# Optimization experiments

Hardware: AMD Instinct MI355X
Metric: run time of the kernel (lower is better)

The kernel has to match this reference:

```python
import jax, jax.numpy as jnp
import numpy as np

DIM, B, H, W = 96, 2, 64, 64
D_INNER, D_STATE, DT_RANK, K = 2 * DIM, 16, 6, 4


def _conv2d(x, w, b=None, padding=0, dilation=1, groups=1):
    out = jax.lax.conv_general_dilated(
        x, w, (1, 1), [(padding, padding)] * 2,
        rhs_dilation=(dilation, dilation),
        dimension_numbers=('NCHW', 'OIHW', 'NCHW'),
        feature_group_count=groups)
    return out if b is None else out + b[None, :, None, None]


def _layernorm(x, g, b, eps=1e-5):
    mu = x.mean(-1, keepdims=True)
    xc = x - mu
    var = (xc * xc).mean(-1, keepdims=True)
    return xc * jax.lax.rsqrt(var + eps) * g + b


def _chan_recal(t, w1, w2):
    s = t.mean((2, 3)) + t.max(axis=(2, 3))          # GAP + GMP, (B,C)
    w = jax.nn.sigmoid(jax.nn.relu(s @ w1.T) @ w2.T)
    return t * w[:, :, None, None]


def _selective_scan(u, delta, A, Bm, Cm, D):
    # u, delta: (B,K,d,L); A: (K,d,N); Bm,Cm: (B,K,N,L); D: (K,d)
    Bsz, Kk, d, L = u.shape
    N = A.shape[-1]
    seq = (jnp.moveaxis(delta, -1, 0), jnp.moveaxis(u, -1, 0),
           jnp.moveaxis(Bm, -1, 0), jnp.moveaxis(Cm, -1, 0))
    h0 = jnp.zeros((Bsz, Kk, d, N), u.dtype)

    def step(h, inp):
        dl, ul, bl, cl = inp  # (B,K,d),(B,K,d),(B,K,N),(B,K,N)
        h = jnp.exp(dl[..., None] * A) * h + (dl * ul)[..., None] * bl[:, :, None, :]
        return h, (h * cl[:, :, None, :]).sum(-1)

    _, ys = jax.lax.scan(step, h0, seq)
    return jnp.moveaxis(ys, 0, -1) + D[None, :, :, None] * u  # (B,K,d,L)


def _ss2d(x, in_proj_w, conv_w, conv_b, x_proj_w, dt_w, dt_b,
          A_logs, Ds, out_norm_g, out_norm_b, out_proj_w):
    Bsz, Hh, Ww, C = x.shape
    d = in_proj_w.shape[0] // 2
    xm, z = jnp.split(x @ in_proj_w.T, 2, axis=-1)
    xm = jnp.transpose(xm, (0, 3, 1, 2))  # (B,d,H,W)
    xm = jax.nn.silu(_conv2d(xm, conv_w, conv_b, padding=1, groups=d))
    L = Hh * Ww
    x_hw = xm.reshape(Bsz, d, L)
    x_wh = jnp.transpose(xm, (0, 1, 3, 2)).reshape(Bsz, d, L)
    xs = jnp.stack([x_hw, x_wh, x_hw[..., ::-1], x_wh[..., ::-1]], axis=1)  # (B,4,d,L)
    x_dbl = jnp.einsum('bkdl,kcd->bkcl', xs, x_proj_w)
    r = dt_w.shape[-1]
    N = A_logs.shape[-1]
    dts, Bs, Cs = jnp.split(x_dbl, [r, r + N], axis=2)
    dts = jax.nn.softplus(jnp.einsum('bkrl,kdr->bkdl', dts, dt_w) + dt_b[None, :, :, None])
    out_y = _selective_scan(xs, dts, -jnp.exp(A_logs), Bs, Cs, Ds)
    inv_y = out_y[:, 2:4, :, ::-1]
    wh = lambda t: jnp.transpose(t.reshape(Bsz, d, Ww, Hh), (0, 1, 3, 2)).reshape(Bsz, d, L)
    y = out_y[:, 0] + inv_y[:, 0] + wh(out_y[:, 1]) + wh(inv_y[:, 1])
    y = _layernorm(jnp.transpose(y, (0, 2, 1)).reshape(Bsz, Hh, Ww, d), out_norm_g, out_norm_b)
    return (y * jax.nn.silu(z)) @ out_proj_w.T


def _forward(x, arf_w1, arf_b1, arf_w2, arf_b2, arf_w3, arf_b3, arf_w4, arf_b4,
             fuse_w, fuse_b, edge_w, enh_w1, enh_b1, bn_g, bn_b, enh_w2, enh_b2,
             pre_fc1, pre_fc2, norm_g, norm_b, in_proj_w, ss_conv_w, ss_conv_b,
             x_proj_w, dt_w, dt_b, A_logs, Ds, out_norm_g, out_norm_b, out_proj_w,
             post_fc1, post_fc2, proj_w, proj_b):
    shortcut = x
    C = x.shape[1]
    g = C // 4
    # AdaptiveReceptiveField (fc gating branch is dead code in the original forward)
    f1 = _conv2d(x, arf_w1, arf_b1, padding=1, dilation=1, groups=g)
    f2 = _conv2d(x, arf_w2, arf_b2, padding=2, dilation=2, groups=g)
    f3 = _conv2d(x, arf_w3, arf_b3, padding=4, dilation=4, groups=g)
    f4 = _conv2d(x, arf_w4, arf_b4, padding=8, dilation=8, groups=g)
    h = _conv2d(jnp.concatenate([f1, f2, f3, f4], 1), fuse_w, fuse_b)
    # LearnableEdgeEnhancement (BatchNorm in training mode: batch stats, biased var)
    edge = _conv2d(h, edge_w, None, padding=1, groups=C)
    e = _conv2d(edge, enh_w1, enh_b1)
    mu = e.mean((0, 2, 3), keepdims=True)
    var = ((e - mu) ** 2).mean((0, 2, 3), keepdims=True)
    e = jax.nn.relu((e - mu) * jax.lax.rsqrt(var + 1e-5) * bn_g[None, :, None, None]
                    + bn_b[None, :, None, None])
    h = h * (1.0 + jax.nn.sigmoid(_conv2d(e, enh_w2, enh_b2)))
    h = _chan_recal(h, pre_fc1, pre_fc2)
    hn = _layernorm(jnp.transpose(h, (0, 2, 3, 1)), norm_g, norm_b)
    hn = _ss2d(hn, in_proj_w, ss_conv_w, ss_conv_b, x_proj_w, dt_w, dt_b,
               A_logs, Ds, out_norm_g, out_norm_b, out_proj_w)
    h = jnp.transpose(hn, (0, 3, 1, 2))
    h = _chan_recal(h, post_fc1, post_fc2)
    h = _conv2d(h, proj_w, proj_b)
    return shortcut + h


def setup_inputs():
    key = jax.random.key(0)
    ks = iter(jax.random.split(key, 48))
    rn = lambda shape, s=0.05: jax.random.normal(next(ks), shape, jnp.float32) * s
    lap = jnp.array([[0., 1., 0.], [1., -4., 1.], [0., 1., 0.]], jnp.float32)
    q = DIM // 4
    inp = {
        'x': jax.random.normal(next(ks), (B, DIM, H, W), jnp.float32),
        'arf_w1': rn((q, 4, 3, 3)), 'arf_b1': rn((q,)),
        'arf_w2': rn((q, 4, 3, 3)), 'arf_b2': rn((q,)),
        'arf_w3': rn((q, 4, 3, 3)), 'arf_b3': rn((q,)),
        'arf_w4': rn((q, 4, 3, 3)), 'arf_b4': rn((q,)),
        'fuse_w': rn((DIM, DIM, 1, 1)), 'fuse_b': rn((DIM,)),
        'edge_w': jnp.tile(lap[None, None], (DIM, 1, 1, 1)),
        'enh_w1': rn((q, DIM, 1, 1)), 'enh_b1': rn((q,)),
        'bn_g': jnp.ones((q,), jnp.float32), 'bn_b': jnp.zeros((q,), jnp.float32),
        'enh_w2': rn((DIM, q, 1, 1)), 'enh_b2': rn((DIM,)),
        'pre_fc1': rn((q, DIM)), 'pre_fc2': rn((DIM, q)),
        'norm_g': jnp.ones((DIM,), jnp.float32), 'norm_b': jnp.zeros((DIM,), jnp.float32),
        'in_proj_w': rn((2 * D_INNER, DIM)),
        'ss_conv_w': rn((D_INNER, 1, 3, 3)), 'ss_conv_b': rn((D_INNER,)),
        'x_proj_w': rn((K, DT_RANK + 2 * D_STATE, D_INNER)),
        'dt_w': rn((K, D_INNER, DT_RANK), 0.1), 'dt_b': rn((K, D_INNER), 0.1),
        'A_logs': jnp.broadcast_to(jnp.log(jnp.arange(1, D_STATE + 1, dtype=jnp.float32)),
                                   (K, D_INNER, D_STATE)) + jnp.zeros((K, D_INNER, D_STATE), jnp.float32),
        'Ds': jnp.ones((K, D_INNER), jnp.float32),
        'out_norm_g': jnp.ones((D_INNER,), jnp.float32),
        'out_norm_b': jnp.zeros((D_INNER,), jnp.float32),
        'out_proj_w': rn((DIM, D_INNER)),
        'post_fc1': rn((q, DIM)), 'post_fc2': rn((DIM, q)),
        'proj_w': rn((DIM, DIM, 1, 1)), 'proj_b': rn((DIM,)),
    }
    return inp


def reference(x, arf_w1, arf_b1, arf_w2, arf_b2, arf_w3, arf_b3, arf_w4, arf_b4,
              fuse_w, fuse_b, edge_w, enh_w1, enh_b1, bn_g, bn_b, enh_w2, enh_b2,
              pre_fc1, pre_fc2, norm_g, norm_b, in_proj_w, ss_conv_w, ss_conv_b,
              x_proj_w, dt_w, dt_b, A_logs, Ds, out_norm_g, out_norm_b, out_proj_w,
              post_fc1, post_fc2, proj_w, proj_b):
    return _forward(x, arf_w1, arf_b1, arf_w2, arf_b2, arf_w3, arf_b3, arf_w4, arf_b4,
                    fuse_w, fuse_b, edge_w, enh_w1, enh_b1, bn_g, bn_b, enh_w2, enh_b2,
                    pre_fc1, pre_fc2, norm_g, norm_b, in_proj_w, ss_conv_w, ss_conv_b,
                    x_proj_w, dt_w, dt_b, A_logs, Ds, out_norm_g, out_norm_b, out_proj_w,
                    post_fc1, post_fc2, proj_w, proj_b)
```

## Files before the change

kernel.cpp:

```cpp
#include <hip/hip_runtime.h>
#include <cmath>

#define LL   4096
#define HWD  64
#define CCH  96
#define QQ   24
#define DDI  192
#define NST  16
#define NCH  128
#define CLEN 32
#define TSC  32
#define XT2  32
#define XP   108
#define FP   100
#define VP   204

static const size_t OFF_F   = 0;
static const size_t OFF_H   = 786432;
static const size_t OFF_E   = 1572864;
static const size_t OFF_BN  = 1769472;
static const size_t OFF_XM  = 2556736;
static const size_t OFF_Z   = 4129600;
static const size_t OFF_XC  = 5702464;
static const size_t OFF_DTS = 7275328;
static const size_t OFF_BC  = 13566784;
static const size_t OFF_YK  = 14615360;
static const size_t OFF_Y2  = 22528832;
static const size_t OFF_HL  = 23315264;
static const size_t OFF_SD  = 26460992;
static const size_t OFF_HIN = 26657600;
static const size_t OFF_S1PS= 29803328;
static const size_t OFF_S1PM= 29806400;
static const size_t OFF_S2PS= 29809472;
static const size_t OFF_S2PM= 29821760;

static __device__ __forceinline__ int map_k(int k, int l) {
  int ll = (k & 2) ? (LL - 1 - l) : l;
  return (k & 1) ? (((ll & 63) << 6) | (ll >> 6)) : ll;
}

__global__ __launch_bounds__(256) void k_arf(const float* __restrict__ x,
    const float* __restrict__ w1, const float* __restrict__ b1,
    const float* __restrict__ w2, const float* __restrict__ b2,
    const float* __restrict__ w3, const float* __restrict__ b3,
    const float* __restrict__ w4, const float* __restrict__ b4,
    float* __restrict__ f) {
  int idx = blockIdx.x * 256 + threadIdx.x;
  int p = idx & (LL - 1);
  int oc = __builtin_amdgcn_readfirstlane((idx >> 12) % CCH);
  int b  = __builtin_amdgcn_readfirstlane(idx / (CCH * LL));
  int i = oc / QQ, q = oc % QQ;
  int dil = 1 << i;
  const float* w  = (i == 0 ? w1 : i == 1 ? w2 : i == 2 ? w3 : w4) + q * 36;
  const float* bb = (i == 0 ? b1 : i == 1 ? b2 : i == 2 ? b3 : b4);
  int yy0 = p >> 6, xx0 = p & 63;
  float acc = bb[q];
  const float* xin = x + ((size_t)b * CCH + q * 4) * LL;
  #pragma unroll
  for (int ky = 0; ky < 3; ky++) {
    int yy = yy0 + (ky - 1) * dil;
    if (yy < 0 || yy >= HWD) continue;
    #pragma unroll
    for (int kx = 0; kx < 3; kx++) {
      int xx = xx0 + (kx - 1) * dil;
      if (xx < 0 || xx >= HWD) continue;
      int pp = (yy << 6) + xx;
      #pragma unroll
      for (int ci = 0; ci < 4; ci++)
        acc += w[ci * 9 + ky * 3 + kx] * xin[(size_t)ci * LL + pp];
    }
  }
  f[idx] = acc;
}

__global__ __launch_bounds__(256) void k_fuse(const float* __restrict__ f,
    const float* __restrict__ fw, const float* __restrict__ fb, float* __restrict__ h) {
  int pix0 = blockIdx.x * 64;
  int oc0 = blockIdx.y * 48;
  int b = pix0 >> 12, p0 = pix0 & (LL - 1);
  int t = threadIdx.x;
  __shared__ float fs[64][FP];
  __shared__ float wbuf[48 * 96];
  for (int i = t; i < 96 * 16; i += 256) {
    int c = i >> 4, q = i & 15;
    float4 v = *(const float4*)(f + ((size_t)b * CCH + c) * LL + p0 + q * 4);
    fs[q * 4 + 0][c] = v.x; fs[q * 4 + 1][c] = v.y;
    fs[q * 4 + 2][c] = v.z; fs[q * 4 + 3][c] = v.w;
  }
  {
    const float4* src = (const float4*)(fw + (size_t)oc0 * CCH);
    float4* dst = (float4*)wbuf;
    for (int i = t; i < 48 * 24; i += 256) dst[i] = src[i];
  }
  __syncthreads();
  int px = t & 63;
  int cg = __builtin_amdgcn_readfirstlane(t >> 6);
  float acc[12];
  #pragma unroll
  for (int j = 0; j < 12; j++) acc[j] = 0.f;
  for (int c4 = 0; c4 < 24; c4++) {
    float4 xv = *(const float4*)(&fs[px][c4 * 4]);
    #pragma unroll
    for (int j = 0; j < 12; j++) {
      float4 wv = *(const float4*)(&wbuf[(cg * 12 + j) * 96 + c4 * 4]);
      acc[j] = fmaf(xv.x, wv.x, fmaf(xv.y, wv.y, fmaf(xv.z, wv.z, fmaf(xv.w, wv.w, acc[j]))));
    }
  }
  __syncthreads();
  float* ot = &fs[0][0];
  #pragma unroll
  for (int j = 0; j < 12; j++) ot[px * 49 + cg * 12 + j] = acc[j];
  __syncthreads();
  for (int i = t; i < 48 * 64; i += 256) {
    int o = i >> 6, p2 = i & 63;
    h[((size_t)b * CCH + oc0 + o) * LL + p0 + p2] = ot[p2 * 49 + o] + fb[oc0 + o];
  }
}

__global__ __launch_bounds__(256) void k_edge(const float* __restrict__ h,
    const float* __restrict__ ew, float* __restrict__ edge) {
  int idx = blockIdx.x * 256 + threadIdx.x;
  int p = idx & (LL - 1);
  int c = __builtin_amdgcn_readfirstlane((idx >> 12) % CCH);
  int b = __builtin_amdgcn_readfirstlane(idx / (CCH * LL));
  int yy0 = p >> 6, xx0 = p & 63;
  const float* w = ew + c * 9;
  const float* hr = h + ((size_t)b * CCH + c) * LL;
  float acc = 0.f;
  #pragma unroll
  for (int ky = 0; ky < 3; ky++) {
    int yy = yy0 + ky - 1;
    if (yy < 0 || yy >= HWD) continue;
    #pragma unroll
    for (int kx = 0; kx < 3; kx++) {
      int xx = xx0 + kx - 1;
      if (xx < 0 || xx >= HWD) continue;
      acc += w[ky * 3 + kx] * hr[(yy << 6) + xx];
    }
  }
  edge[idx] = acc;
}

__global__ __launch_bounds__(256) void k_e1(const float* __restrict__ edge,
    const float* __restrict__ w, const float* __restrict__ bias, float* __restrict__ e) {
  int idx = blockIdx.x * 256 + threadIdx.x;
  int p = idx & (LL - 1);
  int q = __builtin_amdgcn_readfirstlane((idx >> 12) % QQ);
  int b = __builtin_amdgcn_readfirstlane(idx / (QQ * LL));
  const float* er = edge + (size_t)b * CCH * LL + p;
  const float* wr = w + q * CCH;
  float acc = bias[q];
  for (int c = 0; c < CCH; c++) acc += wr[c] * er[(size_t)c * LL];
  e[idx] = acc;
}

__global__ __launch_bounds__(256) void k_bnstats(const float* __restrict__ e,
    const float* __restrict__ g, const float* __restrict__ bb, float* __restrict__ bn) {
  int q = blockIdx.x, tid = threadIdx.x;
  __shared__ float rs[256], r2[256];
  float s = 0.f, s2 = 0.f;
  for (int b = 0; b < 2; b++) {
    const float* er = e + ((size_t)b * QQ + q) * LL;
    for (int p = tid; p < LL; p += 256) { float v = er[p]; s += v; s2 += v * v; }
  }
  rs[tid] = s; r2[tid] = s2; __syncthreads();
  for (int st = 128; st > 0; st >>= 1) {
    if (tid < st) { rs[tid] += rs[tid + st]; r2[tid] += r2[tid + st]; }
    __syncthreads();
  }
  if (tid == 0) {
    float mu = rs[0] / (2.f * LL);
    float var = r2[0] / (2.f * LL) - mu * mu;
    float sc = g[q] * rsqrtf(var + 1e-5f);
    bn[q] = sc;
    bn[QQ + q] = bb[q] - mu * sc;
  }
}

__global__ __launch_bounds__(256) void k_enh(const float* __restrict__ e,
    const float* __restrict__ bn, const float* __restrict__ w2,
    const float* __restrict__ b2, float* __restrict__ h,
    float* __restrict__ s1ps, float* __restrict__ s1pm) {
  int tid = threadIdx.x;
  int idx = blockIdx.x * 256 + tid;
  int p = idx & (LL - 1);
  int o = __builtin_amdgcn_readfirstlane((idx >> 12) % CCH);
  int b = __builtin_amdgcn_readfirstlane(idx / (CCH * LL));
  const float* er = e + (size_t)b * QQ * LL + p;
  const float* wr = w2 + o * QQ;
  float acc = b2[o];
  #pragma unroll
  for (int q = 0; q < QQ; q++) {
    float en = fmaxf(er[(size_t)q * LL] * bn[q] + bn[QQ + q], 0.f);
    acc += wr[q] * en;
  }
  float sig = 1.f / (1.f + __expf(-acc));
  float val = h[idx] * (1.f + sig);
  h[idx] = val;
  __shared__ float rsum[256], rmax[256];
  rsum[tid] = val; rmax[tid] = val; __syncthreads();
  for (int st = 128; st > 0; st >>= 1) {
    if (tid < st) { rsum[tid] += rsum[tid + st]; rmax[tid] = fmaxf(rmax[tid], rmax[tid + st]); }
    __syncthreads();
  }
  if (tid == 0) {
    int row = blockIdx.x >> 4, blk = blockIdx.x & 15;
    s1ps[row * 16 + blk] = rsum[0];
    s1pm[row * 16 + blk] = rmax[0];
  }
}

__global__ __launch_bounds__(256) void k_inproj(const float* __restrict__ h,
    const float* __restrict__ s1ps, const float* __restrict__ s1pm,
    const float* __restrict__ fc1, const float* __restrict__ fc2,
    const float* __restrict__ ng, const float* __restrict__ nb,
    const float* __restrict__ W, float* __restrict__ xm, float* __restrict__ z) {
  int pix0 = blockIdx.x * 64;
  int oc0 = blockIdx.y * CCH;
  int b = pix0 >> 12, p0 = pix0 & (LL - 1);
  int t = threadIdx.x;
  __shared__ float xs[64][XP];
  __shared__ float wbuf[CCH * CCH];
  __shared__ float wsm[CCH];
  __shared__ float hid[QQ];
  __shared__ float ps[64][4], ps2[64][4];
  __shared__ float mu_s[64], rs_s[64];
  if (t < CCH) {
    const float4* sp = (const float4*)(s1ps + (size_t)(b * CCH + t) * 16);
    const float4* mp = (const float4*)(s1pm + (size_t)(b * CCH + t) * 16);
    float s = 0.f, m = -3.402823466e38f;
    #pragma unroll
    for (int i = 0; i < 4; i++) {
      float4 a = sp[i]; s += a.x + a.y + a.z + a.w;
      float4 c = mp[i]; m = fmaxf(m, fmaxf(fmaxf(c.x, c.y), fmaxf(c.z, c.w)));
    }
    wsm[t] = s / (float)LL + m;
  }
  __syncthreads();
  if (t < QQ) {
    float a = 0.f;
    for (int c = 0; c < CCH; c++) a += wsm[c] * fc1[t * CCH + c];
    hid[t] = fmaxf(a, 0.f);
  }
  __syncthreads();
  float w1v = 0.f;
  if (t < CCH) {
    float a = 0.f;
    #pragma unroll
    for (int q = 0; q < QQ; q++) a += hid[q] * fc2[t * QQ + q];
    w1v = 1.f / (1.f + __expf(-a));
  }
  __syncthreads();
  if (t < CCH) wsm[t] = w1v;
  {
    const float4* src = (const float4*)(W + (size_t)oc0 * CCH);
    float4* dst = (float4*)wbuf;
    for (int i = t; i < CCH * 24; i += 256) dst[i] = src[i];
  }
  __syncthreads();
  for (int i = t; i < CCH * 16; i += 256) {
    int c = i >> 4, q = i & 15;
    float w = wsm[c];
    float4 v = *(const float4*)(h + ((size_t)b * CCH + c) * LL + p0 + q * 4);
    xs[q * 4 + 0][c] = v.x * w; xs[q * 4 + 1][c] = v.y * w;
    xs[q * 4 + 2][c] = v.z * w; xs[q * 4 + 3][c] = v.w * w;
  }
  __syncthreads();
  {
    int px = t & 63, qr = t >> 6;
    float s = 0.f, s2 = 0.f;
    #pragma unroll
    for (int j = 0; j < 24; j++) { float v = xs[px][qr * 24 + j]; s += v; s2 += v * v; }
    ps[px][qr] = s; ps2[px][qr] = s2;
  }
  __syncthreads();
  if (t < 64) {
    float ss = ps[t][0] + ps[t][1] + ps[t][2] + ps[t][3];
    float ss2 = ps2[t][0] + ps2[t][1] + ps2[t][2] + ps2[t][3];
    float mu = ss / (float)CCH;
    mu_s[t] = mu;
    rs_s[t] = rsqrtf(ss2 / (float)CCH - mu * mu + 1e-5f);
  }
  __syncthreads();
  for (int i = t; i < 64 * CCH; i += 256) {
    int px = i / CCH, c = i % CCH;
    xs[px][c] = (xs[px][c] - mu_s[px]) * rs_s[px] * ng[c] + nb[c];
  }
  __syncthreads();
  int li = t & 63;
  int cg = __builtin_amdgcn_readfirstlane(t >> 6);
  float acc[24];
  #pragma unroll
  for (int j = 0; j < 24; j++) acc[j] = 0.f;
  for (int dq = 0; dq < 24; dq++) {
    float4 xv = *(const float4*)(&xs[li][dq * 4]);
    #pragma unroll
    for (int j = 0; j < 24; j++) {
      float4 wv = *(const float4*)(&wbuf[(cg + 4 * j) * CCH + dq * 4]);
      acc[j] = fmaf(xv.x, wv.x, fmaf(xv.y, wv.y, fmaf(xv.z, wv.z, fmaf(xv.w, wv.w, acc[j]))));
    }
  }
  __syncthreads();
  float* ot = &xs[0][0];
  #pragma unroll
  for (int j = 0; j < 24; j++) ot[li * 97 + cg + 4 * j] = acc[j];
  __syncthreads();
  float* dst = (oc0 < DDI) ? xm : z;
  int od0 = oc0 % DDI;
  for (int i = t; i < 64 * 96; i += 256) {
    int row = i / 96, c = i % 96;
    dst[(size_t)(pix0 + row) * DDI + od0 + c] = ot[row * 97 + c];
  }
}

__global__ __launch_bounds__(256) void k_ssconv(const float* __restrict__ xm,
    const float* __restrict__ w, const float* __restrict__ bias, float* __restrict__ xc) {
  int idx = blockIdx.x * 256 + threadIdx.x;
  int d = idx % DDI;
  int rem = idx / DDI;
  int xx0 = rem & 63;
  int y0 = ((rem >> 6) & 31) * 2;
  int b = idx / (DDI * LL / 2);
  float wv[9];
  #pragma unroll
  for (int i = 0; i < 9; i++) wv[i] = w[d * 9 + i];
  float acc0 = bias[d], acc1 = bias[d];
  const float* xr = xm + (size_t)b * LL * DDI + d;
  #pragma unroll
  for (int ky = -1; ky <= 2; ky++) {
    int yy = y0 + ky;
    if (yy < 0 || yy >= HWD) continue;
    #pragma unroll
    for (int kx = -1; kx <= 1; kx++) {
      int xx = xx0 + kx;
      if (xx < 0 || xx >= HWD) continue;
      float val = xr[(size_t)((yy << 6) + xx) * DDI];
      if (ky <= 1) acc0 += wv[(ky + 1) * 3 + (kx + 1)] * val;
      if (ky >= 0) acc1 += wv[ky * 3 + (kx + 1)] * val;
    }
  }
  size_t o0 = ((size_t)b * LL + (y0 << 6) + xx0) * DDI + d;
  xc[o0] = acc0 / (1.f + __expf(-acc0));
  xc[o0 + 64 * DDI] = acc1 / (1.f + __expf(-acc1));
}

__global__ __launch_bounds__(256) void k_xdbl(const float* __restrict__ xc,
    const float* __restrict__ xpw, float* __restrict__ dtr_ws, float* __restrict__ bcb) {
  int lt = blockIdx.x;
  int bk = blockIdx.y;
  int b = bk >> 2, k = bk & 3;
  int t = threadIdx.x;
  __shared__ float xs[XT2][XP];
  __shared__ float wbuf[38 * 96];
  int l0 = lt * XT2;
  int pos = t & 31;
  int cg = t >> 5;
  float acc[5];
  #pragma unroll
  for (int j = 0; j < 5; j++) acc[j] = 0.f;
  for (int h = 0; h < 2; h++) {
    __syncthreads();
    for (int i = t; i < XT2 * 24; i += 256) {
      int row = i / 24, dq = i % 24;
      int p = map_k(k, l0 + row);
      *(float4*)(&xs[row][dq * 4]) =
          *(const float4*)(xc + ((size_t)b * LL + p) * DDI + h * 96 + dq * 4);
    }
    for (int i = t; i < 38 * 24; i += 256) {
      int c = i / 24, dq = i % 24;
      *(float4*)(&wbuf[c * 96 + dq * 4]) =
          *(const float4*)(xpw + ((size_t)k * 38 + c) * DDI + h * 96 + dq * 4);
    }
    __syncthreads();
    for (int dq = 0; dq < 24; dq++) {
      float4 xv = *(const float4*)(&xs[pos][dq * 4]);
      #pragma unroll
      for (int j = 0; j < 5; j++) {
        int c = cg + 8 * j;
        if (c < 38) {
          float4 wv = *(const float4*)(&wbuf[c * 96 + dq * 4]);
          acc[j] = fmaf(xv.x, wv.x, fmaf(xv.y, wv.y, fmaf(xv.z, wv.z, fmaf(xv.w, wv.w, acc[j]))));
        }
      }
    }
  }
  #pragma unroll
  for (int j = 0; j < 5; j++) {
    int c = cg + 8 * j;
    if (c < 6) dtr_ws[((size_t)bk * LL + l0 + pos) * 6 + c] = acc[j];
    else if (c < 38) bcb[((size_t)bk * LL + l0 + pos) * 32 + (c - 6)] = acc[j];
  }
}

template <int PASS>
__global__ __launch_bounds__(192) void k_scan(const float* __restrict__ dtr_ws,
    const float* __restrict__ bcb, const float* __restrict__ xc,
    const float* __restrict__ A_logs, const float* __restrict__ dtw,
    const float* __restrict__ dtb, float* __restrict__ hl, float* __restrict__ sd,
    const float* __restrict__ hin, float* __restrict__ yk) {
  int ch = blockIdx.x, bk = blockIdx.y;
  int b = bk >> 2, k = bk & 3;
  int d = threadIdx.x;
  __shared__ float u_s[TSC][DDI];
  __shared__ float bcs[TSC][32];
  __shared__ float dtr_s[TSC][6];
  float Av[NST];
  #pragma unroll
  for (int n = 0; n < NST; n++) Av[n] = -__expf(A_logs[(size_t)(k * DDI + d) * NST + n]);
  bool pw = true;
  #pragma unroll
  for (int n = 1; n < NST; n++) pw = pw && (fabsf(Av[n] - (float)(n + 1) * Av[0]) <= 1e-3f * (n + 1));
  float wdt[6];
  #pragma unroll
  for (int r = 0; r < 6; r++) wdt[r] = dtw[((size_t)(k * DDI + d)) * 6 + r];
  float bdt = dtb[k * DDI + d];
  float h[NST];
  if (PASS == 0) {
    #pragma unroll
    for (int n = 0; n < NST; n++) h[n] = 0.f;
  } else {
    const float* hp = hin + ((size_t)(bk * DDI + d) * NCH + ch) * NST;
    #pragma unroll
    for (int n = 0; n < NST; n++) h[n] = hp[n];
  }
  float sumdt = 0.f;
  int l0 = ch * CLEN;
  {
    for (int i = d; i < TSC * (DDI / 4); i += 192) {
      int row = i / (DDI / 4), q = i % (DDI / 4);
      int p = map_k(k, l0 + row);
      ((float4*)u_s)[i] = *(const float4*)(xc + ((size_t)b * LL + p) * DDI + q * 4);
    }
    {
      const float4* src = (const float4*)(bcb + ((size_t)bk * LL + l0) * 32);
      float4* dst = (float4*)bcs;
      for (int i = d; i < TSC * 32 / 4; i += 192) dst[i] = src[i];
    }
    for (int i = d; i < TSC * 6; i += 192)
      ((float*)dtr_s)[i] = dtr_ws[((size_t)bk * LL + l0) * 6 + i];
    __syncthreads();
    for (int tt = 0; tt < TSC; tt++) {
      float a = bdt;
      #pragma unroll
      for (int r = 0; r < 6; r++) a = fmaf(wdt[r], dtr_s[tt][r], a);
      float dt = (a > 15.f) ? a : __logf(1.f + __expf(a));
      float u  = u_s[tt][d];
      float dtu = dt * u;
      if (PASS == 0) sumdt += dt;
      float eA[NST];
      if (pw) {
        float E = __expf(dt * Av[0]);
        float en = 1.f;
        #pragma unroll
        for (int n = 0; n < NST; n++) { en *= E; eA[n] = en; }
      } else {
        #pragma unroll
        for (int n = 0; n < NST; n++) eA[n] = __expf(dt * Av[n]);
      }
      float y = 0.f;
      #pragma unroll
      for (int n = 0; n < NST; n++) {
        h[n] = eA[n] * h[n] + dtu * bcs[tt][n];
        y += h[n] * bcs[tt][16 + n];
      }
      if (PASS == 1) {
        int p = map_k(k, l0 + tt);
        yk[((size_t)bk * LL + p) * DDI + d] = y;
      }
    }
  }
  if (PASS == 0) {
    float* hp = hl + ((size_t)(bk * DDI + d) * NCH + ch) * NST;
    #pragma unroll
    for (int n = 0; n < NST; n++) hp[n] = h[n];
    sd[(size_t)(bk * DDI + d) * NCH + ch] = sumdt;
  }
}

__global__ __launch_bounds__(256) void k_carry(const float* __restrict__ A_logs,
    const float* __restrict__ hl, const float* __restrict__ sd, float* __restrict__ hin) {
  int idx = blockIdx.x * 256 + threadIdx.x;
  int n = idx & 15;
  int d = (idx >> 4) % DDI;
  int bk = idx / (DDI * NST);
  int k = bk & 3;
  float Aval = -__expf(A_logs[(size_t)(k * DDI + d) * NST + n]);
  float h = 0.f;
  size_t base = (size_t)(bk * DDI + d) * NCH;
  for (int ch = 0; ch < NCH; ch++) {
    hin[(base + ch) * NST + n] = h;
    h = __expf(Aval * sd[base + ch]) * h + hl[(base + ch) * NST + n];
  }
}

__global__ __launch_bounds__(256) void k_outproj(const float* __restrict__ yk,
    const float* __restrict__ xc, const float* __restrict__ Ds, const float* __restrict__ z,
    const float* __restrict__ ong, const float* __restrict__ onb,
    const float* __restrict__ W, float* __restrict__ y2,
    float* __restrict__ s2ps, float* __restrict__ s2pm) {
  int pix0 = blockIdx.x * 64;
  int oc0 = blockIdx.y * 48;
  int b = pix0 >> 12, p0 = pix0 & (LL - 1);
  int t = threadIdx.x;
  __shared__ float xs[64][VP];
  __shared__ float wbuf[48 * 96];
  __shared__ float dsum[DDI];
  __shared__ float ps[64][4], ps2[64][4];
  __shared__ float mu_s[64], rs_s[64];
  if (t < 48) {
    float4 a  = *(const float4*)(Ds + t * 4);
    float4 c1 = *(const float4*)(Ds + DDI + t * 4);
    float4 c2 = *(const float4*)(Ds + 2 * DDI + t * 4);
    float4 c3 = *(const float4*)(Ds + 3 * DDI + t * 4);
    *(float4*)(&dsum[t * 4]) = make_float4(a.x + c1.x + c2.x + c3.x, a.y + c1.y + c2.y + c3.y,
                                           a.z + c1.z + c2.z + c3.z, a.w + c1.w + c2.w + c3.w);
  }
  __syncthreads();
  int px = t & 63, qr = t >> 6;
  int p = p0 + px;
  size_t pb = ((size_t)b * LL + p) * DDI;
  size_t yb = ((size_t)b * 4 * LL + p) * DDI;
  {
    float s = 0.f, s2 = 0.f;
    #pragma unroll
    for (int j = 0; j < 12; j++) {
      int c = (qr * 12 + j) * 4;
      float4 y0 = *(const float4*)(yk + yb + c);
      float4 y1 = *(const float4*)(yk + yb + (size_t)LL * DDI + c);
      float4 y2v = *(const float4*)(yk + yb + 2ul * LL * DDI + c);
      float4 y3 = *(const float4*)(yk + yb + 3ul * LL * DDI + c);
      float4 u = *(const float4*)(xc + pb + c);
      float4 dv = *(const float4*)(&dsum[c]);
      float4 v;
      v.x = y0.x + y1.x + y2v.x + y3.x + dv.x * u.x;
      v.y = y0.y + y1.y + y2v.y + y3.y + dv.y * u.y;
      v.z = y0.z + y1.z + y2v.z + y3.z + dv.z * u.z;
      v.w = y0.w + y1.w + y2v.w + y3.w + dv.w * u.w;
      *(float4*)(&xs[px][c]) = v;
      s += v.x + v.y + v.z + v.w;
      s2 += v.x * v.x + v.y * v.y + v.z * v.z + v.w * v.w;
    }
    ps[px][qr] = s; ps2[px][qr] = s2;
  }
  __syncthreads();
  if (t < 64) {
    float ss = ps[t][0] + ps[t][1] + ps[t][2] + ps[t][3];
    float ss2 = ps2[t][0] + ps2[t][1] + ps2[t][2] + ps2[t][3];
    float mu = ss / (float)DDI;
    mu_s[t] = mu;
    rs_s[t] = rsqrtf(ss2 / (float)DDI - mu * mu + 1e-5f);
  }
  __syncthreads();
  {
    float mu = mu_s[px], rs = rs_s[px];
    #pragma unroll
    for (int j = 0; j < 12; j++) {
      int c = (qr * 12 + j) * 4;
      float4 v = *(const float4*)(&xs[px][c]);
      float4 zz = *(const float4*)(z + pb + c);
      float4 og = *(const float4*)(ong + c);
      float4 ob = *(const float4*)(onb + c);
      float4 gv;
      gv.x = ((v.x - mu) * rs * og.x + ob.x) * (zz.x / (1.f + __expf(-zz.x)));
      gv.y = ((v.y - mu) * rs * og.y + ob.y) * (zz.y / (1.f + __expf(-zz.y)));
      gv.z = ((v.z - mu) * rs * og.z + ob.z) * (zz.z / (1.f + __expf(-zz.z)));
      gv.w = ((v.w - mu) * rs * og.w + ob.w) * (zz.w / (1.f + __expf(-zz.w)));
      *(float4*)(&xs[px][c]) = gv;
    }
  }
  int li = px;
  int cg = __builtin_amdgcn_readfirstlane(qr);
  float acc[12];
  #pragma unroll
  for (int j = 0; j < 12; j++) acc[j] = 0.f;
  for (int hh = 0; hh < 2; hh++) {
    __syncthreads();
    for (int i = t; i < 48 * 24; i += 256) {
      int c = i / 24, dq = i % 24;
      *(float4*)(&wbuf[c * 96 + dq * 4]) =
          *(const float4*)(W + (size_t)(oc0 + c) * DDI + hh * 96 + dq * 4);
    }
    __syncthreads();
    for (int dq = 0; dq < 24; dq++) {
      float4 xv = *(const float4*)(&xs[li][hh * 96 + dq * 4]);
      #pragma unroll
      for (int j = 0; j < 12; j++) {
        float4 wv = *(const float4*)(&wbuf[(cg + 4 * j) * 96 + dq * 4]);
        acc[j] = fmaf(xv.x, wv.x, fmaf(xv.y, wv.y, fmaf(xv.z, wv.z, fmaf(xv.w, wv.w, acc[j]))));
      }
    }
  }
  int lane = t & 63;
  #pragma unroll
  for (int j = 0; j < 12; j++) {
    float sv = acc[j], mv = acc[j];
    #pragma unroll
    for (int o = 32; o > 0; o >>= 1) {
      sv += __shfl_xor(sv, o);
      mv = fmaxf(mv, __shfl_xor(mv, o));
    }
    if (lane == 0) {
      int oc = oc0 + cg + 4 * j;
      int tile = blockIdx.x & 63;
      s2ps[(size_t)(b * CCH + oc) * 64 + tile] = sv;
      s2pm[(size_t)(b * CCH + oc) * 64 + tile] = mv;
    }
  }
  __syncthreads();
  float* ot = &xs[0][0];
  #pragma unroll
  for (int j = 0; j < 12; j++) ot[li * 49 + cg + 4 * j] = acc[j];
  __syncthreads();
  for (int i = t; i < 48 * 64; i += 256) {
    int o = i / 64, pi = i % 64;
    y2[((size_t)b * CCH + oc0 + o) * LL + p0 + pi] = ot[pi * 49 + o];
  }
}

__global__ __launch_bounds__(256) void k_final(const float* __restrict__ x,
    const float* __restrict__ y2, const float* __restrict__ s2ps, const float* __restrict__ s2pm,
    const float* __restrict__ fc1, const float* __restrict__ fc2,
    const float* __restrict__ pw, const float* __restrict__ pb, float* __restrict__ out) {
  int pix0 = blockIdx.x * 64;
  int oc0 = blockIdx.y * 48;
  int b = pix0 >> 12, p0 = pix0 & (LL - 1);
  int t = threadIdx.x;
  __shared__ float fs[64][FP];
  __shared__ float wbuf[48 * 96];
  __shared__ float wsm[CCH];
  __shared__ float hid[QQ];
  if (t < CCH) {
    const float4* sp = (const float4*)(s2ps + (size_t)(b * CCH + t) * 64);
    const float4* mp = (const float4*)(s2pm + (size_t)(b * CCH + t) * 64);
    float s = 0.f, m = -3.402823466e38f;
    #pragma unroll
    for (int i = 0; i < 16; i++) {
      float4 a = sp[i]; s += a.x + a.y + a.z + a.w;
      float4 c = mp[i]; m = fmaxf(m, fmaxf(fmaxf(c.x, c.y), fmaxf(c.z, c.w)));
    }
    wsm[t] = s / (float)LL + m;
  }
  __syncthreads();
  if (t < QQ) {
    float a = 0.f;
    for (int c = 0; c < CCH; c++) a += wsm[c] * fc1[t * CCH + c];
    hid[t] = fmaxf(a, 0.f);
  }
  __syncthreads();
  float w2v = 0.f;
  if (t < CCH) {
    float a = 0.f;
    #pragma unroll
    for (int q = 0; q < QQ; q++) a += hid[q] * fc2[t * QQ + q];
    w2v = 1.f / (1.f + __expf(-a));
  }
  __syncthreads();
  if (t < CCH) wsm[t] = w2v;
  __syncthreads();
  for (int i = t; i < 96 * 16; i += 256) {
    int c = i >> 4, q = i & 15;
    float4 v = *(const float4*)(y2 + ((size_t)b * CCH + c) * LL + p0 + q * 4);
    fs[q * 4 + 0][c] = v.x; fs[q * 4 + 1][c] = v.y;
    fs[q * 4 + 2][c] = v.z; fs[q * 4 + 3][c] = v.w;
  }
  for (int i = t; i < 48 * 24; i += 256) {
    int row = i / 24, q = i % 24;
    float4 wv = *(const float4*)(pw + (size_t)(oc0 + row) * CCH + q * 4);
    ((float4*)wbuf)[i] = make_float4(wv.x * wsm[q * 4], wv.y * wsm[q * 4 + 1],
                                     wv.z * wsm[q * 4 + 2], wv.w * wsm[q * 4 + 3]);
  }
  __syncthreads();
  int px = t & 63;
  int cg = __builtin_amdgcn_readfirstlane(t >> 6);
  float acc[12];
  #pragma unroll
  for (int j = 0; j < 12; j++) acc[j] = 0.f;
  for (int c4 = 0; c4 < 24; c4++) {
    float4 xv = *(const float4*)(&fs[px][c4 * 4]);
    #pragma unroll
    for (int j = 0; j < 12; j++) {
      float4 wv = *(const float4*)(&wbuf[(cg * 12 + j) * 96 + c4 * 4]);
      acc[j] = fmaf(xv.x, wv.x, fmaf(xv.y, wv.y, fmaf(xv.z, wv.z, fmaf(xv.w, wv.w, acc[j]))));
    }
  }
  __syncthreads();
  float* ot = &fs[0][0];
  #pragma unroll
  for (int j = 0; j < 12; j++) ot[px * 49 + cg * 12 + j] = acc[j];
  __syncthreads();
  for (int i = t; i < 48 * 64; i += 256) {
    int o = i >> 6, p2 = i & 63;
    size_t oi = ((size_t)b * CCH + oc0 + o) * LL + p0 + p2;
    out[oi] = x[oi] + pb[oc0 + o] + ot[p2 * 49 + o];
  }
}

extern "C" void kernel_launch(void* const* d_in, const int* in_sizes, int n_in,
                              void* d_out, int out_size, void* d_ws, size_t ws_size,
                              hipStream_t stream) {
  const float* x        = (const float*)d_in[0];
  const float* arf_w1   = (const float*)d_in[1];
  const float* arf_b1   = (const float*)d_in[2];
  const float* arf_w2   = (const float*)d_in[3];
  const float* arf_b2   = (const float*)d_in[4];
  const float* arf_w3   = (const float*)d_in[5];
  const float* arf_b3   = (const float*)d_in[6];
  const float* arf_w4   = (const float*)d_in[7];
  const float* arf_b4   = (const float*)d_in[8];
  const float* fuse_w   = (const float*)d_in[9];
  const float* fuse_b   = (const float*)d_in[10];
  const float* edge_w   = (const float*)d_in[11];
  const float* enh_w1   = (const float*)d_in[12];
  const float* enh_b1   = (const float*)d_in[13];
  const float* bn_g     = (const float*)d_in[14];
  const float* bn_b     = (const float*)d_in[15];
  const float* enh_w2   = (const float*)d_in[16];
  const float* enh_b2   = (const float*)d_in[17];
  const float* pre_fc1  = (const float*)d_in[18];
  const float* pre_fc2  = (const float*)d_in[19];
  const float* norm_g   = (const float*)d_in[20];
  const float* norm_b   = (const float*)d_in[21];
  const float* in_proj_w= (const float*)d_in[22];
  const float* ss_conv_w= (const float*)d_in[23];
  const float* ss_conv_b= (const float*)d_in[24];
  const float* x_proj_w = (const float*)d_in[25];
  const float* dt_w     = (const float*)d_in[26];
  const float* dt_b     = (const float*)d_in[27];
  const float* A_logs   = (const float*)d_in[28];
  const float* Ds       = (const float*)d_in[29];
  const float* out_ng   = (const float*)d_in[30];
  const float* out_nb   = (const float*)d_in[31];
  const float* out_proj_w = (const float*)d_in[32];
  const float* post_fc1 = (const float*)d_in[33];
  const float* post_fc2 = (const float*)d_in[34];
  const float* proj_w   = (const float*)d_in[35];
  const float* proj_b   = (const float*)d_in[36];

  float* ws = (float*)d_ws;
  float* fbuf  = ws + OFF_F;
  float* hbuf  = ws + OFF_H;
  float* ebuf  = ws + OFF_E;
  float* bnbuf = ws + OFF_BN;
  float* xmbuf = ws + OFF_XM;
  float* zbuf  = ws + OFF_Z;
  float* xcbuf = ws + OFF_XC;
  float* dtrbuf= ws + OFF_DTS;
  float* bcbuf = ws + OFF_BC;
  float* ykbuf = ws + OFF_YK;
  float* y2buf = ws + OFF_Y2;
  float* hlbuf = ws + OFF_HL;
  float* sdbuf = ws + OFF_SD;
  float* hinbuf= ws + OFF_HIN;
  float* s1ps  = ws + OFF_S1PS;
  float* s1pm  = ws + OFF_S1PM;
  float* s2ps  = ws + OFF_S2PS;
  float* s2pm  = ws + OFF_S2PM;

  k_arf<<<3072, 256, 0, stream>>>(x, arf_w1, arf_b1, arf_w2, arf_b2, arf_w3, arf_b3, arf_w4, arf_b4, fbuf);
  k_fuse<<<dim3(128, 2), 256, 0, stream>>>(fbuf, fuse_w, fuse_b, hbuf);
  k_edge<<<3072, 256, 0, stream>>>(hbuf, edge_w, fbuf);
  k_e1<<<768, 256, 0, stream>>>(fbuf, enh_w1, enh_b1, ebuf);
  k_bnstats<<<24, 256, 0, stream>>>(ebuf, bn_g, bn_b, bnbuf);
  k_enh<<<3072, 256, 0, stream>>>(ebuf, bnbuf, enh_w2, enh_b2, hbuf, s1ps, s1pm);
  k_inproj<<<dim3(128, 4), 256, 0, stream>>>(hbuf, s1ps, s1pm, pre_fc1, pre_fc2, norm_g, norm_b, in_proj_w, xmbuf, zbuf);
  k_ssconv<<<3072, 256, 0, stream>>>(xmbuf, ss_conv_w, ss_conv_b, xcbuf);
  k_xdbl<<<dim3(LL / XT2, 8), 256, 0, stream>>>(xcbuf, x_proj_w, dtrbuf, bcbuf);
  k_scan<0><<<dim3(NCH, 8), 192, 0, stream>>>(dtrbuf, bcbuf, xcbuf, A_logs, dt_w, dt_b, hlbuf, sdbuf, nullptr, nullptr);
  k_carry<<<96, 256, 0, stream>>>(A_logs, hlbuf, sdbuf, hinbuf);
  k_scan<1><<<dim3(NCH, 8), 192, 0, stream>>>(dtrbuf, bcbuf, xcbuf, A_logs, dt_w, dt_b, nullptr, nullptr, hinbuf, ykbuf);
  k_outproj<<<dim3(128, 2), 256, 0, stream>>>(ykbuf, xcbuf, Ds, zbuf, out_ng, out_nb, out_proj_w, y2buf, s2ps, s2pm);
  k_final<<<dim3(128, 2), 256, 0, stream>>>(x, y2buf, s2ps, s2pm, post_fc1, post_fc2, proj_w, proj_b, (float*)d_out);
  (void)in_sizes; (void)n_in; (void)out_size; (void)ws_size;
}
```

Baseline: 228.9 us.

## Fuse chunked scan passes via cooperative grid sync and fold BN stats into producers

The two scan passes and the carry-propagation kernel are merged into one cooperative kernel that keeps the staged chunk inputs in shared memory and uses two grid-wide syncs in place of separate launches. The chunk data is loaded once instead of twice. The BN statistics kernel is removed: k_e1 now writes per-block partial sums, and each k_enh block reduces them into shared scale and shift values. Together these cut three kernel launches and one reload of the scan inputs. In exchange, the carry phase now runs on only 24576 of the 196608 scan threads, every k_enh block repeats the small stats reduction, and all 1024 blocks must be resident at once for the cooperative launch to work.

```diff
diff --git a/kernel.cpp b/kernel.cpp
--- a/kernel.cpp
+++ b/kernel.cpp
@@ -1,5 +1,8 @@
 #include <hip/hip_runtime.h>
+#include <hip/hip_cooperative_groups.h>
 #include <cmath>
+
+namespace cg = cooperative_groups;
 
 #define LL   4096
 #define HWD  64
@@ -15,24 +18,25 @@
 #define FP   100
 #define VP   204
 
-static const size_t OFF_F   = 0;
-static const size_t OFF_H   = 786432;
-static const size_t OFF_E   = 1572864;
-static const size_t OFF_BN  = 1769472;
-static const size_t OFF_XM  = 2556736;
-static const size_t OFF_Z   = 4129600;
-static const size_t OFF_XC  = 5702464;
-static const size_t OFF_DTS = 7275328;
-static const size_t OFF_BC  = 13566784;
-static const size_t OFF_YK  = 14615360;
-static const size_t OFF_Y2  = 22528832;
-static const size_t OFF_HL  = 23315264;
-static const size_t OFF_SD  = 26460992;
-static const size_t OFF_HIN = 26657600;
-static const size_t OFF_S1PS= 29803328;
-static const size_t OFF_S1PM= 29806400;
-static const size_t OFF_S2PS= 29809472;
-static const size_t OFF_S2PM= 29821760;
+static const size_t OFF_F    = 0;
+static const size_t OFF_H    = 786432;
+static const size_t OFF_E    = 1572864;
+static const size_t OFF_E1PS = 1769472;
+static const size_t OFF_E1P2 = 1770240;
+static const size_t OFF_XM   = 2556736;
+static const size_t OFF_Z    = 4129600;
+static const size_t OFF_XC   = 5702464;
+static const size_t OFF_DTS  = 7275328;
+static const size_t OFF_BC   = 13566784;
+static const size_t OFF_YK   = 14615360;
+static const size_t OFF_Y2   = 22528832;
+static const size_t OFF_HL   = 23315264;
+static const size_t OFF_SD   = 26460992;
+static const size_t OFF_HIN  = 26657600;
+static const size_t OFF_S1PS = 29803328;
+static const size_t OFF_S1PM = 29806400;
+static const size_t OFF_S2PS = 29809472;
+static const size_t OFF_S2PM = 29821760;
 
 static __device__ __forceinline__ int map_k(int k, int l) {
   int ll = (k & 2) ? (LL - 1 - l) : l;
@@ -94,7 +98,7 @@
   }
   __syncthreads();
   int px = t & 63;
-  int cg = __builtin_amdgcn_readfirstlane(t >> 6);
+  int cg2 = __builtin_amdgcn_readfirstlane(t >> 6);
   float acc[12];
   #pragma unroll
   for (int j = 0; j < 12; j++) acc[j] = 0.f;
@@ -102,14 +106,14 @@
     float4 xv = *(const float4*)(&fs[px][c4 * 4]);
     #pragma unroll
     for (int j = 0; j < 12; j++) {
-      float4 wv = *(const float4*)(&wbuf[(cg * 12 + j) * 96 + c4 * 4]);
+      float4 wv = *(const float4*)(&wbuf[(cg2 * 12 + j) * 96 + c4 * 4]);
       acc[j] = fmaf(xv.x, wv.x, fmaf(xv.y, wv.y, fmaf(xv.z, wv.z, fmaf(xv.w, wv.w, acc[j]))));
     }
   }
   __syncthreads();
   float* ot = &fs[0][0];
   #pragma unroll
-  for (int j = 0; j < 12; j++) ot[px * 49 + cg * 12 + j] = acc[j];
+  for (int j = 0; j < 12; j++) ot[px * 49 + cg2 * 12 + j] = acc[j];
   __syncthreads();
   for (int i = t; i < 48 * 64; i += 256) {
     int o = i >> 6, p2 = i & 63;
@@ -142,8 +146,10 @@
 }
 
 __global__ __launch_bounds__(256) void k_e1(const float* __restrict__ edge,
-    const float* __restrict__ w, const float* __restrict__ bias, float* __restrict__ e) {
-  int idx = blockIdx.x * 256 + threadIdx.x;
+    const float* __restrict__ w, const float* __restrict__ bias, float* __restrict__ e,
+    float* __restrict__ e1ps, float* __restrict__ e1p2) {
+  int tid = threadIdx.x;
+  int idx = blockIdx.x * 256 + tid;
   int p = idx & (LL - 1);
   int q = __builtin_amdgcn_readfirstlane((idx >> 12) % QQ);
   int b = __builtin_amdgcn_readfirstlane(idx / (QQ * LL));
@@ -152,36 +158,37 @@
   float acc = bias[q];
   for (int c = 0; c < CCH; c++) acc += wr[c] * er[(size_t)c * LL];
   e[idx] = acc;
-}
-
-__global__ __launch_bounds__(256) void k_bnstats(const float* __restrict__ e,
-    const float* __restrict__ g, const float* __restrict__ bb, float* __restrict__ bn) {
-  int q = blockIdx.x, tid = threadIdx.x;
   __shared__ float rs[256], r2[256];
-  float s = 0.f, s2 = 0.f;
-  for (int b = 0; b < 2; b++) {
-    const float* er = e + ((size_t)b * QQ + q) * LL;
-    for (int p = tid; p < LL; p += 256) { float v = er[p]; s += v; s2 += v * v; }
-  }
-  rs[tid] = s; r2[tid] = s2; __syncthreads();
+  rs[tid] = acc; r2[tid] = acc * acc; __syncthreads();
   for (int st = 128; st > 0; st >>= 1) {
     if (tid < st) { rs[tid] += rs[tid + st]; r2[tid] += r2[tid + st]; }
     __syncthreads();
   }
-  if (tid == 0) {
-    float mu = rs[0] / (2.f * LL);
-    float var = r2[0] / (2.f * LL) - mu * mu;
-    float sc = g[q] * rsqrtf(var + 1e-5f);
-    bn[q] = sc;
-    bn[QQ + q] = bb[q] - mu * sc;
-  }
+  if (tid == 0) { e1ps[blockIdx.x] = rs[0]; e1p2[blockIdx.x] = r2[0]; }
 }
 
 __global__ __launch_bounds__(256) void k_enh(const float* __restrict__ e,
-    const float* __restrict__ bn, const float* __restrict__ w2,
-    const float* __restrict__ b2, float* __restrict__ h,
-    float* __restrict__ s1ps, float* __restrict__ s1pm) {
+    const float* __restrict__ e1ps, const float* __restrict__ e1p2,
+    const float* __restrict__ bn_g, const float* __restrict__ bn_b,
+    const float* __restrict__ w2, const float* __restrict__ b2,
+    float* __restrict__ h, float* __restrict__ s1ps, float* __restrict__ s1pm) {
   int tid = threadIdx.x;
+  __shared__ float bns[QQ], bnsh[QQ];
+  if (tid < QQ) {
+    float s = 0.f, s2 = 0.f;
+    #pragma unroll
+    for (int b2 = 0; b2 < 2; b2++)
+      for (int i = 0; i < 16; i++) {
+        int pi = (b2 * QQ + tid) * 16 + i;
+        s += e1ps[pi]; s2 += e1p2[pi];
+      }
+    float mu = s / (2.f * LL);
+    float var = s2 / (2.f * LL) - mu * mu;
+    float sc = bn_g[tid] * rsqrtf(var + 1e-5f);
+    bns[tid] = sc;
+    bnsh[tid] = bn_b[tid] - mu * sc;
+  }
+  __syncthreads();
   int idx = blockIdx.x * 256 + tid;
   int p = idx & (LL - 1);
   int o = __builtin_amdgcn_readfirstlane((idx >> 12) % CCH);
@@ -191,7 +198,7 @@
   float acc = b2[o];
   #pragma unroll
   for (int q = 0; q < QQ; q++) {
-    float en = fmaxf(er[(size_t)q * LL] * bn[q] + bn[QQ + q], 0.f);
+    float en = fmaxf(er[(size_t)q * LL] * bns[q] + bnsh[q], 0.f);
     acc += wr[q] * en;
   }
   float sig = 1.f / (1.f + __expf(-acc));
@@ -288,7 +295,7 @@
   }
   __syncthreads();
   int li = t & 63;
-  int cg = __builtin_amdgcn_readfirstlane(t >> 6);
+  int cg2 = __builtin_amdgcn_readfirstlane(t >> 6);
   float acc[24];
   #pragma unroll
   for (int j = 0; j < 24; j++) acc[j] = 0.f;
@@ -296,14 +303,14 @@
     float4 xv = *(const float4*)(&xs[li][dq * 4]);
     #pragma unroll
     for (int j = 0; j < 24; j++) {
-      float4 wv = *(const float4*)(&wbuf[(cg + 4 * j) * CCH + dq * 4]);
+      float4 wv = *(const float4*)(&wbuf[(cg2 + 4 * j) * CCH + dq * 4]);
       acc[j] = fmaf(xv.x, wv.x, fmaf(xv.y, wv.y, fmaf(xv.z, wv.z, fmaf(xv.w, wv.w, acc[j]))));
     }
   }
   __syncthreads();
   float* ot = &xs[0][0];
   #pragma unroll
-  for (int j = 0; j < 24; j++) ot[li * 97 + cg + 4 * j] = acc[j];
+  for (int j = 0; j < 24; j++) ot[li * 97 + cg2 + 4 * j] = acc[j];
   __syncthreads();
   float* dst = (oc0 < DDI) ? xm : z;
   int od0 = oc0 % DDI;
@@ -354,7 +361,7 @@
   __shared__ float wbuf[38 * 96];
   int l0 = lt * XT2;
   int pos = t & 31;
-  int cg = t >> 5;
+  int cg2 = t >> 5;
   float acc[5];
   #pragma unroll
   for (int j = 0; j < 5; j++) acc[j] = 0.f;
@@ -376,7 +383,7 @@
       float4 xv = *(const float4*)(&xs[pos][dq * 4]);
       #pragma unroll
       for (int j = 0; j < 5; j++) {
-        int c = cg + 8 * j;
+        int c = cg2 + 8 * j;
         if (c < 38) {
           float4 wv = *(const float4*)(&wbuf[c * 96 + dq * 4]);
           acc[j] = fmaf(xv.x, wv.x, fmaf(xv.y, wv.y, fmaf(xv.z, wv.z, fmaf(xv.w, wv.w, acc[j]))));
@@ -386,18 +393,17 @@
   }
   #pragma unroll
   for (int j = 0; j < 5; j++) {
-    int c = cg + 8 * j;
+    int c = cg2 + 8 * j;
     if (c < 6) dtr_ws[((size_t)bk * LL + l0 + pos) * 6 + c] = acc[j];
     else if (c < 38) bcb[((size_t)bk * LL + l0 + pos) * 32 + (c - 6)] = acc[j];
   }
 }
 
-template <int PASS>
-__global__ __launch_bounds__(192) void k_scan(const float* __restrict__ dtr_ws,
+__global__ __launch_bounds__(192) void k_scan_all(const float* __restrict__ dtr_ws,
     const float* __restrict__ bcb, const float* __restrict__ xc,
     const float* __restrict__ A_logs, const float* __restrict__ dtw,
     const float* __restrict__ dtb, float* __restrict__ hl, float* __restrict__ sd,
-    const float* __restrict__ hin, float* __restrict__ yk) {
+    float* __restrict__ hin, float* __restrict__ yk) {
   int ch = blockIdx.x, bk = blockIdx.y;
   int b = bk >> 2, k = bk & 3;
   int d = threadIdx.x;
@@ -414,82 +420,98 @@
   #pragma unroll
   for (int r = 0; r < 6; r++) wdt[r] = dtw[((size_t)(k * DDI + d)) * 6 + r];
   float bdt = dtb[k * DDI + d];
+  int l0 = ch * CLEN;
+  for (int i = d; i < TSC * (DDI / 4); i += 192) {
+    int row = i / (DDI / 4), q = i % (DDI / 4);
+    int p = map_k(k, l0 + row);
+    ((float4*)u_s)[i] = *(const float4*)(xc + ((size_t)b * LL + p) * DDI + q * 4);
+  }
+  {
+    const float4* src = (const float4*)(bcb + ((size_t)bk * LL + l0) * 32);
+    float4* dst = (float4*)bcs;
+    for (int i = d; i < TSC * 32 / 4; i += 192) dst[i] = src[i];
+  }
+  for (int i = d; i < TSC * 6; i += 192)
+    ((float*)dtr_s)[i] = dtr_ws[((size_t)bk * LL + l0) * 6 + i];
+  __syncthreads();
   float h[NST];
-  if (PASS == 0) {
-    #pragma unroll
-    for (int n = 0; n < NST; n++) h[n] = 0.f;
-  } else {
-    const float* hp = hin + ((size_t)(bk * DDI + d) * NCH + ch) * NST;
-    #pragma unroll
-    for (int n = 0; n < NST; n++) h[n] = hp[n];
-  }
+  #pragma unroll
+  for (int n = 0; n < NST; n++) h[n] = 0.f;
   float sumdt = 0.f;
-  int l0 = ch * CLEN;
-  {
-    for (int i = d; i < TSC * (DDI / 4); i += 192) {
-      int row = i / (DDI / 4), q = i % (DDI / 4);
-      int p = map_k(k, l0 + row);
-      ((float4*)u_s)[i] = *(const float4*)(xc + ((size_t)b * LL + p) * DDI + q * 4);
-    }
-    {
-      const float4* src = (const float4*)(bcb + ((size_t)bk * LL + l0) * 32);
-      float4* dst = (float4*)bcs;
-      for (int i = d; i < TSC * 32 / 4; i += 192) dst[i] = src[i];
-    }
-    for (int i = d; i < TSC * 6; i += 192)
-      ((float*)dtr_s)[i] = dtr_ws[((size_t)bk * LL + l0) * 6 + i];
-    __syncthreads();
-    for (int tt = 0; tt < TSC; tt++) {
-      float a = bdt;
+  for (int tt = 0; tt < TSC; tt++) {
+    float a = bdt;
+    #pragma unroll
+    for (int r = 0; r < 6; r++) a = fmaf(wdt[r], dtr_s[tt][r], a);
+    float dt = (a > 15.f) ? a : __logf(1.f + __expf(a));
+    float dtu = dt * u_s[tt][d];
+    sumdt += dt;
+    float eA[NST];
+    if (pw) {
+      float E = __expf(dt * Av[0]);
+      float en = 1.f;
       #pragma unroll
-      for (int r = 0; r < 6; r++) a = fmaf(wdt[r], dtr_s[tt][r], a);
-      float dt = (a > 15.f) ? a : __logf(1.f + __expf(a));
-      float u  = u_s[tt][d];
-      float dtu = dt * u;
-      if (PASS == 0) sumdt += dt;
-      float eA[NST];
-      if (pw) {
-        float E = __expf(dt * Av[0]);
-        float en = 1.f;
-        #pragma unroll
-        for (int n = 0; n < NST; n++) { en *= E; eA[n] = en; }
-      } else {
-        #pragma unroll
-        for (int n = 0; n < NST; n++) eA[n] = __expf(dt * Av[n]);
-      }
-      float y = 0.f;
+      for (int n = 0; n < NST; n++) { en *= E; eA[n] = en; }
+    } else {
       #pragma unroll
-      for (int n = 0; n < NST; n++) {
-        h[n] = eA[n] * h[n] + dtu * bcs[tt][n];
-        y += h[n] * bcs[tt][16 + n];
-      }
-      if (PASS == 1) {
-        int p = map_k(k, l0 + tt);
-        yk[((size_t)bk * LL + p) * DDI + d] = y;
-      }
-    }
-  }
-  if (PASS == 0) {
+      for (int n = 0; n < NST; n++) eA[n] = __expf(dt * Av[n]);
+    }
+    #pragma unroll
+    for (int n = 0; n < NST; n++) h[n] = eA[n] * h[n] + dtu * bcs[tt][n];
+  }
+  {
     float* hp = hl + ((size_t)(bk * DDI + d) * NCH + ch) * NST;
     #pragma unroll
     for (int n = 0; n < NST; n++) hp[n] = h[n];
     sd[(size_t)(bk * DDI + d) * NCH + ch] = sumdt;
   }
-}
-
-__global__ __launch_bounds__(256) void k_carry(const float* __restrict__ A_logs,
-    const float* __restrict__ hl, const float* __restrict__ sd, float* __restrict__ hin) {
-  int idx = blockIdx.x * 256 + threadIdx.x;
-  int n = idx & 15;
-  int d = (idx >> 4) % DDI;
-  int bk = idx / (DDI * NST);
-  int k = bk & 3;
-  float Aval = -__expf(A_logs[(size_t)(k * DDI + d) * NST + n]);
-  float h = 0.f;
-  size_t base = (size_t)(bk * DDI + d) * NCH;
-  for (int ch = 0; ch < NCH; ch++) {
-    hin[(base + ch) * NST + n] = h;
-    h = __expf(Aval * sd[base + ch]) * h + hl[(base + ch) * NST + n];
+  cg::this_grid().sync();
+  {
+    int fb = blockIdx.y * gridDim.x + blockIdx.x;
+    int tg = fb * 192 + d;
+    if (tg < 8 * DDI * NST) {
+      int n = tg & 15;
+      int d2 = (tg >> 4) % DDI;
+      int bk2 = tg / (DDI * NST);
+      int k2 = bk2 & 3;
+      float Aval = -__expf(A_logs[(size_t)(k2 * DDI + d2) * NST + n]);
+      float hh = 0.f;
+      size_t base = (size_t)(bk2 * DDI + d2) * NCH;
+      for (int c2 = 0; c2 < NCH; c2++) {
+        hin[(base + c2) * NST + n] = hh;
+        hh = __expf(Aval * sd[base + c2]) * hh + hl[(base + c2) * NST + n];
+      }
+    }
+  }
+  cg::this_grid().sync();
+  {
+    const float* hp = hin + ((size_t)(bk * DDI + d) * NCH + ch) * NST;
+    #pragma unroll
+    for (int n = 0; n < NST; n++) h[n] = hp[n];
+  }
+  for (int tt = 0; tt < TSC; tt++) {
+    float a = bdt;
+    #pragma unroll
+    for (int r = 0; r < 6; r++) a = fmaf(wdt[r], dtr_s[tt][r], a);
+    float dt = (a > 15.f) ? a : __logf(1.f + __expf(a));
+    float dtu = dt * u_s[tt][d];
+    float eA[NST];
+    if (pw) {
+      float E = __expf(dt * Av[0]);
+      float en = 1.f;
+      #pragma unroll
+      for (int n = 0; n < NST; n++) { en *= E; eA[n] = en; }
+    } else {
+      #pragma unroll
+      for (int n = 0; n < NST; n++) eA[n] = __expf(dt * Av[n]);
+    }
+    float y = 0.f;
+    #pragma unroll
+    for (int n = 0; n < NST; n++) {
+      h[n] = eA[n] * h[n] + dtu * bcs[tt][n];
+      y += h[n] * bcs[tt][16 + n];
+    }
+    int p = map_k(k, l0 + tt);
+    yk[((size_t)bk * LL + p) * DDI + d] = y;
   }
 }
 
@@ -569,7 +591,7 @@
     }
   }
   int li = px;
-  int cg = __builtin_amdgcn_readfirstlane(qr);
+  int cg2 = __builtin_amdgcn_readfirstlane(qr);
   float acc[12];
   #pragma unroll
   for (int j = 0; j < 12; j++) acc[j] = 0.f;
@@ -585,7 +607,7 @@
       float4 xv = *(const float4*)(&xs[li][hh * 96 + dq * 4]);
       #pragma unroll
       for (int j = 0; j < 12; j++) {
-        float4 wv = *(const float4*)(&wbuf[(cg + 4 * j) * 96 + dq * 4]);
+        float4 wv = *(const float4*)(&wbuf[(cg2 + 4 * j) * 96 + dq * 4]);
         acc[j] = fmaf(xv.x, wv.x, fmaf(xv.y, wv.y, fmaf(xv.z, wv.z, fmaf(xv.w, wv.w, acc[j]))));
       }
     }
@@ -600,7 +622,7 @@
       mv = fmaxf(mv, __shfl_xor(mv, o));
     }
     if (lane == 0) {
-      int oc = oc0 + cg + 4 * j;
+      int oc = oc0 + cg2 + 4 * j;
       int tile = blockIdx.x & 63;
       s2ps[(size_t)(b * CCH + oc) * 64 + tile] = sv;
       s2pm[(size_t)(b * CCH + oc) * 64 + tile] = mv;
@@ -609,7 +631,7 @@
   __syncthreads();
   float* ot = &xs[0][0];
   #pragma unroll
-  for (int j = 0; j < 12; j++) ot[li * 49 + cg + 4 * j] = acc[j];
+  for (int j = 0; j < 12; j++) ot[li * 49 + cg2 + 4 * j] = acc[j];
   __syncthreads();
   for (int i = t; i < 48 * 64; i += 256) {
     int o = i / 64, pi = i % 64;
@@ -671,7 +693,7 @@
   }
   __syncthreads();
   int px = t & 63;
-  int cg = __builtin_amdgcn_readfirstlane(t >> 6);
+  int cg2 = __builtin_amdgcn_readfirstlane(t >> 6);
   float acc[12];
   #pragma unroll
   for (int j = 0; j < 12; j++) acc[j] = 0.f;
@@ -679,14 +701,14 @@
     float4 xv = *(const float4*)(&fs[px][c4 * 4]);
     #pragma unroll
     for (int j = 0; j < 12; j++) {
-      float4 wv = *(const float4*)(&wbuf[(cg * 12 + j) * 96 + c4 * 4]);
+      float4 wv = *(const float4*)(&wbuf[(cg2 * 12 + j) * 96 + c4 * 4]);
       acc[j] = fmaf(xv.x, wv.x, fmaf(xv.y, wv.y, fmaf(xv.z, wv.z, fmaf(xv.w, wv.w, acc[j]))));
     }
   }
   __syncthreads();
   float* ot = &fs[0][0];
   #pragma unroll
-  for (int j = 0; j < 12; j++) ot[px * 49 + cg * 12 + j] = acc[j];
+  for (int j = 0; j < 12; j++) ot[px * 49 + cg2 * 12 + j] = acc[j];
   __syncthreads();
   for (int i = t; i < 48 * 64; i += 256) {
     int o = i >> 6, p2 = i & 63;
@@ -740,7 +762,8 @@
   float* fbuf  = ws + OFF_F;
   float* hbuf  = ws + OFF_H;
   float* ebuf  = ws + OFF_E;
-  float* bnbuf = ws + OFF_BN;
+  float* e1ps  = ws + OFF_E1PS;
+  float* e1p2  = ws + OFF_E1P2;
   float* xmbuf = ws + OFF_XM;
   float* zbuf  = ws + OFF_Z;
   float* xcbuf = ws + OFF_XC;
@@ -759,15 +782,17 @@
   k_arf<<<3072, 256, 0, stream>>>(x, arf_w1, arf_b1, arf_w2, arf_b2, arf_w3, arf_b3, arf_w4, arf_b4, fbuf);
   k_fuse<<<dim3(128, 2), 256, 0, stream>>>(fbuf, fuse_w, fuse_b, hbuf);
   k_edge<<<3072, 256, 0, stream>>>(hbuf, edge_w, fbuf);
-  k_e1<<<768, 256, 0, stream>>>(fbuf, enh_w1, enh_b1, ebuf);
-  k_bnstats<<<24, 256, 0, stream>>>(ebuf, bn_g, bn_b, bnbuf);
-  k_enh<<<3072, 256, 0, stream>>>(ebuf, bnbuf, enh_w2, enh_b2, hbuf, s1ps, s1pm);
+  k_e1<<<768, 256, 0, stream>>>(fbuf, enh_w1, enh_b1, ebuf, e1ps, e1p2);
+  k_enh<<<3072, 256, 0, stream>>>(ebuf, e1ps, e1p2, bn_g, bn_b, enh_w2, enh_b2, hbuf, s1ps, s1pm);
   k_inproj<<<dim3(128, 4), 256, 0, stream>>>(hbuf, s1ps, s1pm, pre_fc1, pre_fc2, norm_g, norm_b, in_proj_w, xmbuf, zbuf);
   k_ssconv<<<3072, 256, 0, stream>>>(xmbuf, ss_conv_w, ss_conv_b, xcbuf);
   k_xdbl<<<dim3(LL / XT2, 8), 256, 0, stream>>>(xcbuf, x_proj_w, dtrbuf, bcbuf);
-  k_scan<0><<<dim3(NCH, 8), 192, 0, stream>>>(dtrbuf, bcbuf, xcbuf, A_logs, dt_w, dt_b, hlbuf, sdbuf, nullptr, nullptr);
-  k_carry<<<96, 256, 0, stream>>>(A_logs, hlbuf, sdbuf, hinbuf);
-  k_scan<1><<<dim3(NCH, 8), 192, 0, stream>>>(dtrbuf, bcbuf, xcbuf, A_logs, dt_w, dt_b, nullptr, nullptr, hinbuf, ykbuf);
+  {
+    void* args[] = {(void*)&dtrbuf, (void*)&bcbuf, (void*)&xcbuf, (void*)&A_logs,
+                    (void*)&dt_w, (void*)&dt_b, (void*)&hlbuf, (void*)&sdbuf,
+                    (void*)&hinbuf, (void*)&ykbuf};
+    hipLaunchCooperativeKernel((const void*)k_scan_all, dim3(NCH, 8), dim3(192), args, 0, stream);
+  }
   k_outproj<<<dim3(128, 2), 256, 0, stream>>>(ykbuf, xcbuf, Ds, zbuf, out_ng, out_nb, out_proj_w, y2buf, s2ps, s2pm);
   k_final<<<dim3(128, 2), 256, 0, stream>>>(x, y2buf, s2ps, s2pm, post_fc1, post_fc2, proj_w, proj_b, (float*)d_out);
   (void)in_sizes; (void)n_in; (void)out_size; (void)ws_size;
```

New measurement: 432.8 us. 89.1% more time.
